# Performance work log

Measured on AMD Instinct MI355X. Metric: run time of the kernel, lower is better.

The kernel has to match this reference:

```python
import jax, jax.numpy as jnp
import numpy as np

B = 32768          # batch (replay-buffer minibatch)
OBS, ACT = 17, 6   # HalfCheetah-style dims
IN = OBS + ACT
H = 256            # hidden width hard-coded in the module
N = 10             # num_q_nets


def setup_inputs() -> dict:
    key = jax.random.key(0)
    ks = jax.random.split(key, 8)
    # PyTorch Linear default init: U(-1/sqrt(fan_in), 1/sqrt(fan_in)); scale randn similarly.
    s1, s2, s3 = 1.0 / np.sqrt(IN), 1.0 / np.sqrt(H), 1.0 / np.sqrt(H)
    return {
        "state": jax.random.normal(ks[0], (B, OBS), dtype=jnp.float32),
        "action": jax.random.uniform(ks[1], (B, ACT), dtype=jnp.float32, minval=-1.0, maxval=1.0),
        "W1": jax.random.normal(ks[2], (N, IN, H), dtype=jnp.float32) * s1,
        "b1": jax.random.normal(ks[3], (N, H), dtype=jnp.float32) * s1,
        "W2": jax.random.normal(ks[4], (N, H, H), dtype=jnp.float32) * s2,
        "b2": jax.random.normal(ks[5], (N, H), dtype=jnp.float32) * s2,
        "W3": jax.random.normal(ks[6], (N, H, 1), dtype=jnp.float32) * s3,
        "b3": jax.random.normal(ks[7], (N, 1), dtype=jnp.float32) * s3,
    }


def reference(state, action, W1, b1, W2, b2, W3, b3):
    # x: [B, OBS+ACT]
    x = jnp.concatenate([state, action], axis=1)
    # batched-over-ensemble GEMMs; n=ensemble member, b=batch
    h1 = jax.nn.relu(jnp.einsum("bi,nih->nbh", x, W1) + b1[:, None, :])   # [N,B,H]
    h2 = jax.nn.relu(jnp.einsum("nbh,nho->nbo", h1, W2) + b2[:, None, :])  # [N,B,H]
    out = jnp.einsum("nbh,nho->nbo", h2, W3) + b3[:, None, :]              # [N,B,1]
    return out
```

## Files before the change

### kernel.cpp

```cpp
#include <hip/hip_runtime.h>
#include <hip/hip_bf16.h>


typedef __attribute__((ext_vector_type(8))) short bf16x8;
typedef __attribute__((ext_vector_type(4))) float f32x4;

#define B_TOTAL 32768
#define NQ 10
#define HDIM 256
#define BT 128
#define XS_STRIDE 40

#define W1P_ELEMS (NQ * 16 * 64 * 8)
#define W2P_ELEMS (NQ * 8 * 16 * 64 * 8)

__device__ __forceinline__ unsigned short f2bf(float f) {
  unsigned int u = __float_as_uint(f);
  u = u + 0x7FFFu + ((u >> 16) & 1u);
  return (unsigned short)(u >> 16);
}

__device__ __forceinline__ unsigned int pk2bf(float a, float b) {
  union { __hip_bfloat162 h; unsigned int u; } cv;
  cv.h = __float22bfloat162_rn(make_float2(a, b));
  return cv.u;
}

__global__ void pack_weights_kernel(const float* __restrict__ W1,
                                    const float* __restrict__ W2,
                                    unsigned short* __restrict__ w1p,
                                    unsigned short* __restrict__ w2p) {
  int t = blockIdx.x * 256 + threadIdx.x;
  const int NW1 = NQ * 16 * 64;
  if (t < NW1) {
    int lane = t & 63, mt = (t >> 6) & 15, n = t >> 10;
    int m = lane & 15, q = lane >> 4;
    int outc = mt * 16 + m;
    unsigned short v[8];
#pragma unroll
    for (int j = 0; j < 8; j++) {
      int k = q * 8 + j;
      v[j] = (k < 23) ? f2bf(W1[(n * 23 + k) * 256 + outc]) : (unsigned short)0;
    }
    *(uint4*)&w1p[(size_t)t * 8] = *(const uint4*)v;
  } else {
    int u = t - NW1;
    int lane = u & 63, mt = (u >> 6) & 15, kt = (u >> 10) & 7, n = u >> 13;
    int m = lane & 15, q = lane >> 4;
    int outc = mt * 16 + m;
    unsigned short v[8];
#pragma unroll
    for (int j = 0; j < 8; j++) {
      int h = kt * 32 + q * 8 + j;
      v[j] = f2bf(W2[((size_t)(n * 256 + h)) * 256 + outc]);
    }
    *(uint4*)&w2p[(size_t)u * 8] = *(const uint4*)v;
  }
}

__global__ __launch_bounds__(512, 4) void fused_ensemble_kernel(
    const float* __restrict__ state,
    const float* __restrict__ action,
    const unsigned short* __restrict__ w1p,
    const float* __restrict__ b1,
    const unsigned short* __restrict__ w2p,
    const float* __restrict__ b2,
    const float* __restrict__ W3,
    const float* __restrict__ b3,
    float* __restrict__ out) {
  __shared__ __align__(16) unsigned short xs[BT * XS_STRIDE];
  __shared__ __align__(16) unsigned short hs[32 * BT * 8];

  const int tid = threadIdx.x;
  const int lane = tid & 63;
  const int w = tid >> 6;
  const int m = lane & 15;
  const int q = lane >> 4;

  const int n = blockIdx.x >> 8;
  const int row0 = (blockIdx.x & 255) * BT;

  {
    const float* sp = state + (size_t)row0 * 17;
    for (int i = tid; i < BT * 17; i += 512) {
      int b = i / 17, k = i - b * 17;
      xs[b * XS_STRIDE + k] = f2bf(sp[i]);
    }
    const float* ap = action + (size_t)row0 * 6;
    for (int i = tid; i < BT * 6; i += 512) {
      int b = i / 6, k = i - b * 6;
      xs[b * XS_STRIDE + 17 + k] = f2bf(ap[i]);
    }
    for (int i = tid; i < BT * 9; i += 512) {
      int b = i / 9, k = i - b * 9;
      xs[b * XS_STRIDE + 23 + k] = 0;
    }
  }
  __syncthreads();

  f32x4 acc[2][8];

  {
    bf16x8 af[2];
#pragma unroll
    for (int mt = 0; mt < 2; mt++)
      af[mt] = *(const bf16x8*)(w1p + (((size_t)n * 16 + w * 2 + mt) * 64 + lane) * 8);
#pragma unroll
    for (int mt = 0; mt < 2; mt++) {
      float4 bv = *(const float4*)&b1[n * HDIM + (w * 2 + mt) * 16 + q * 4];
      f32x4 bi = (f32x4){bv.x, bv.y, bv.z, bv.w};
#pragma unroll
      for (int nt = 0; nt < 8; nt++) acc[mt][nt] = bi;
    }
#pragma unroll
    for (int nt = 0; nt < 8; nt++) {
      bf16x8 bfr = *(const bf16x8*)&xs[(nt * 16 + m) * XS_STRIDE + q * 8];
#pragma unroll
      for (int mt = 0; mt < 2; mt++)
        acc[mt][nt] = __builtin_amdgcn_mfma_f32_16x16x32_bf16(af[mt], bfr, acc[mt][nt], 0, 0, 0);
    }
  }

  {
    const int kqb = w * 4 + (q >> 1);
    const int joff = (q & 1) * 4;
#pragma unroll
    for (int mt = 0; mt < 2; mt++)
#pragma unroll
      for (int nt = 0; nt < 8; nt++) {
        f32x4 a = acc[mt][nt];
        uint2 wv;
        wv.x = pk2bf(fmaxf(a[0], 0.f), fmaxf(a[1], 0.f));
        wv.y = pk2bf(fmaxf(a[2], 0.f), fmaxf(a[3], 0.f));
        *(uint2*)&hs[(((kqb + mt * 2) * BT) + nt * 16 + m) * 8 + joff] = wv;
      }
  }
  __syncthreads();

  {
    const unsigned short* w2n = w2p + (size_t)n * (8 * 16 * 64 * 8);
    bf16x8 acur[2], anxt[2];
#pragma unroll
    for (int mt = 0; mt < 2; mt++)
      acur[mt] = *(const bf16x8*)(w2n + (((size_t)(w * 2 + mt)) * 64 + lane) * 8);
#pragma unroll
    for (int mt = 0; mt < 2; mt++) {
      float4 bv = *(const float4*)&b2[n * HDIM + (w * 2 + mt) * 16 + q * 4];
      f32x4 bi = (f32x4){bv.x, bv.y, bv.z, bv.w};
#pragma unroll
      for (int nt = 0; nt < 8; nt++) acc[mt][nt] = bi;
    }
#pragma unroll
    for (int kt = 0; kt < 8; kt++) {
      if (kt < 7) {
#pragma unroll
        for (int mt = 0; mt < 2; mt++)
          anxt[mt] = *(const bf16x8*)(w2n + (((size_t)(kt + 1) * 16 + w * 2 + mt) * 64 + lane) * 8);
      }
#pragma unroll
      for (int half = 0; half < 2; half++) {
        bf16x8 bfr[4];
#pragma unroll
        for (int i = 0; i < 4; i++) {
          int nt = half * 4 + i;
          bfr[i] = *(const bf16x8*)&hs[((kt * 4 + q) * BT + nt * 16 + m) * 8];
        }
#pragma unroll
        for (int i = 0; i < 4; i++)
#pragma unroll
          for (int mt = 0; mt < 2; mt++)
            acc[mt][half * 4 + i] = __builtin_amdgcn_mfma_f32_16x16x32_bf16(
                acur[mt], bfr[i], acc[mt][half * 4 + i], 0, 0, 0);
      }
#pragma unroll
      for (int mt = 0; mt < 2; mt++) acur[mt] = anxt[mt];
    }
  }

  {
    float4 w3v[2];
#pragma unroll
    for (int mt = 0; mt < 2; mt++)
      w3v[mt] = *(const float4*)&W3[n * HDIM + (w * 2 + mt) * 16 + q * 4];
    float p[8];
#pragma unroll
    for (int nt = 0; nt < 8; nt++) {
      float s = 0.f;
#pragma unroll
      for (int mt = 0; mt < 2; mt++) {
        f32x4 a = acc[mt][nt];
        float4 wv = w3v[mt];
        s = fmaf(fmaxf(a[0], 0.f), wv.x, s);
        s = fmaf(fmaxf(a[1], 0.f), wv.y, s);
        s = fmaf(fmaxf(a[2], 0.f), wv.z, s);
        s = fmaf(fmaxf(a[3], 0.f), wv.w, s);
      }
      s += __shfl_xor(s, 16, 64);
      s += __shfl_xor(s, 32, 64);
      p[nt] = s;
    }
    float* red = (float*)xs;
    if (q == 0) {
#pragma unroll
      for (int nt = 0; nt < 8; nt++) red[w * BT + nt * 16 + m] = p[nt];
    }
    __syncthreads();
    if (tid < BT) {
      float s = b3[n];
#pragma unroll
      for (int ww = 0; ww < 8; ww++) s += red[ww * BT + tid];
      out[(size_t)n * B_TOTAL + row0 + tid] = s;
    }
  }
}

extern "C" void kernel_launch(void* const* d_in, const int* in_sizes, int n_in,
                              void* d_out, int out_size, void* d_ws, size_t ws_size,
                              hipStream_t stream) {
  const float* state  = (const float*)d_in[0];
  const float* action = (const float*)d_in[1];
  const float* W1 = (const float*)d_in[2];
  const float* b1 = (const float*)d_in[3];
  const float* W2 = (const float*)d_in[4];
  const float* b2 = (const float*)d_in[5];
  const float* W3 = (const float*)d_in[6];
  const float* b3 = (const float*)d_in[7];
  float* out = (float*)d_out;

  unsigned short* w1p = (unsigned short*)d_ws;
  unsigned short* w2p = (unsigned short*)((char*)d_ws + (size_t)W1P_ELEMS * 2);

  pack_weights_kernel<<<360, 256, 0, stream>>>(W1, W2, w1p, w2p);
  fused_ensemble_kernel<<<NQ * (B_TOTAL / BT), 512, 0, stream>>>(
      state, action, w1p, b1, w2p, b2, W3, b3, out);
}
```

Baseline: 120.8 us.

## Pre-pack inputs to bf16 and retile waves as 4x4 MFMA blocks

```diff
diff --git a/kernel.cpp b/kernel.cpp
--- a/kernel.cpp
+++ b/kernel.cpp
@@ -9,8 +9,8 @@
 #define NQ 10
 #define HDIM 256
 #define BT 128
-#define XS_STRIDE 40
-
+
+#define XP_ELEMS  (B_TOTAL * 32)
 #define W1P_ELEMS (NQ * 16 * 64 * 8)
 #define W2P_ELEMS (NQ * 8 * 16 * 64 * 8)
 
@@ -26,14 +26,36 @@
   return cv.u;
 }
 
-__global__ void pack_weights_kernel(const float* __restrict__ W1,
-                                    const float* __restrict__ W2,
-                                    unsigned short* __restrict__ w1p,
-                                    unsigned short* __restrict__ w2p) {
+__global__ void pack_all_kernel(const float* __restrict__ state,
+                                const float* __restrict__ action,
+                                const float* __restrict__ W1,
+                                const float* __restrict__ W2,
+                                unsigned short* __restrict__ xp,
+                                unsigned short* __restrict__ w1p,
+                                unsigned short* __restrict__ w2p) {
   int t = blockIdx.x * 256 + threadIdx.x;
+  const int NX  = B_TOTAL * 4;
   const int NW1 = NQ * 16 * 64;
-  if (t < NW1) {
-    int lane = t & 63, mt = (t >> 6) & 15, n = t >> 10;
+  if (t < NX) {
+    int b = t >> 2, seg = t & 3;
+    unsigned short v[8];
+    if (seg < 2) {
+      const float* sp = state + (size_t)b * 17 + seg * 8;
+#pragma unroll
+      for (int j = 0; j < 8; j++) v[j] = f2bf(sp[j]);
+    } else if (seg == 2) {
+      v[0] = f2bf(state[(size_t)b * 17 + 16]);
+#pragma unroll
+      for (int j = 0; j < 6; j++) v[1 + j] = f2bf(action[(size_t)b * 6 + j]);
+      v[7] = 0;
+    } else {
+#pragma unroll
+      for (int j = 0; j < 8; j++) v[j] = 0;
+    }
+    *(uint4*)&xp[(size_t)t * 8] = *(const uint4*)v;
+  } else if (t < NX + NW1) {
+    int u = t - NX;
+    int lane = u & 63, mt = (u >> 6) & 15, n = u >> 10;
     int m = lane & 15, q = lane >> 4;
     int outc = mt * 16 + m;
     unsigned short v[8];
@@ -42,9 +64,9 @@
       int k = q * 8 + j;
       v[j] = (k < 23) ? f2bf(W1[(n * 23 + k) * 256 + outc]) : (unsigned short)0;
     }
-    *(uint4*)&w1p[(size_t)t * 8] = *(const uint4*)v;
+    *(uint4*)&w1p[(size_t)u * 8] = *(const uint4*)v;
   } else {
-    int u = t - NW1;
+    int u = t - NX - NW1;
     int lane = u & 63, mt = (u >> 6) & 15, kt = (u >> 10) & 7, n = u >> 13;
     int m = lane & 15, q = lane >> 4;
     int outc = mt * 16 + m;
@@ -59,8 +81,7 @@
 }
 
 __global__ __launch_bounds__(512, 4) void fused_ensemble_kernel(
-    const float* __restrict__ state,
-    const float* __restrict__ action,
+    const unsigned short* __restrict__ xp,
     const unsigned short* __restrict__ w1p,
     const float* __restrict__ b1,
     const unsigned short* __restrict__ w2p,
@@ -68,126 +89,107 @@
     const float* __restrict__ W3,
     const float* __restrict__ b3,
     float* __restrict__ out) {
-  __shared__ __align__(16) unsigned short xs[BT * XS_STRIDE];
   __shared__ __align__(16) unsigned short hs[32 * BT * 8];
+  __shared__ float red[8 * 64];
 
   const int tid = threadIdx.x;
   const int lane = tid & 63;
   const int w = tid >> 6;
   const int m = lane & 15;
   const int q = lane >> 4;
+  const int cg = w >> 1;
+  const int colg = w & 1;
 
   const int n = blockIdx.x >> 8;
   const int row0 = (blockIdx.x & 255) * BT;
 
+  f32x4 acc[4][4];
+
   {
-    const float* sp = state + (size_t)row0 * 17;
-    for (int i = tid; i < BT * 17; i += 512) {
-      int b = i / 17, k = i - b * 17;
-      xs[b * XS_STRIDE + k] = f2bf(sp[i]);
-    }
-    const float* ap = action + (size_t)row0 * 6;
-    for (int i = tid; i < BT * 6; i += 512) {
-      int b = i / 6, k = i - b * 6;
-      xs[b * XS_STRIDE + 17 + k] = f2bf(ap[i]);
-    }
-    for (int i = tid; i < BT * 9; i += 512) {
-      int b = i / 9, k = i - b * 9;
-      xs[b * XS_STRIDE + 23 + k] = 0;
-    }
-  }
-  __syncthreads();
-
-  f32x4 acc[2][8];
-
-  {
-    bf16x8 af[2];
-#pragma unroll
-    for (int mt = 0; mt < 2; mt++)
-      af[mt] = *(const bf16x8*)(w1p + (((size_t)n * 16 + w * 2 + mt) * 64 + lane) * 8);
-#pragma unroll
-    for (int mt = 0; mt < 2; mt++) {
-      float4 bv = *(const float4*)&b1[n * HDIM + (w * 2 + mt) * 16 + q * 4];
+    bf16x8 af[4], bfr[4];
+#pragma unroll
+    for (int nt = 0; nt < 4; nt++) {
+      int col = row0 + colg * 64 + nt * 16 + m;
+      bfr[nt] = *(const bf16x8*)(xp + (size_t)col * 32 + q * 8);
+    }
+#pragma unroll
+    for (int mt = 0; mt < 4; mt++)
+      af[mt] = *(const bf16x8*)(w1p + (((size_t)n * 16 + cg * 4 + mt) * 64 + lane) * 8);
+#pragma unroll
+    for (int mt = 0; mt < 4; mt++) {
+      float4 bv = *(const float4*)&b1[n * HDIM + (cg * 4 + mt) * 16 + q * 4];
       f32x4 bi = (f32x4){bv.x, bv.y, bv.z, bv.w};
 #pragma unroll
-      for (int nt = 0; nt < 8; nt++) acc[mt][nt] = bi;
-    }
-#pragma unroll
-    for (int nt = 0; nt < 8; nt++) {
-      bf16x8 bfr = *(const bf16x8*)&xs[(nt * 16 + m) * XS_STRIDE + q * 8];
-#pragma unroll
-      for (int mt = 0; mt < 2; mt++)
-        acc[mt][nt] = __builtin_amdgcn_mfma_f32_16x16x32_bf16(af[mt], bfr, acc[mt][nt], 0, 0, 0);
-    }
-  }
-
-  {
-    const int kqb = w * 4 + (q >> 1);
-    const int joff = (q & 1) * 4;
-#pragma unroll
-    for (int mt = 0; mt < 2; mt++)
-#pragma unroll
-      for (int nt = 0; nt < 8; nt++) {
-        f32x4 a = acc[mt][nt];
-        uint2 wv;
-        wv.x = pk2bf(fmaxf(a[0], 0.f), fmaxf(a[1], 0.f));
-        wv.y = pk2bf(fmaxf(a[2], 0.f), fmaxf(a[3], 0.f));
-        *(uint2*)&hs[(((kqb + mt * 2) * BT) + nt * 16 + m) * 8 + joff] = wv;
-      }
+      for (int nt = 0; nt < 4; nt++) acc[mt][nt] = bi;
+    }
+#pragma unroll
+    for (int nt = 0; nt < 4; nt++)
+#pragma unroll
+      for (int mt = 0; mt < 4; mt++)
+        acc[mt][nt] = __builtin_amdgcn_mfma_f32_16x16x32_bf16(af[mt], bfr[nt], acc[mt][nt], 0, 0, 0);
+  }
+
+#pragma unroll
+  for (int mt = 0; mt < 4; mt++) {
+    int kq = cg * 8 + mt * 2 + (q >> 1);
+    int joff = (q & 1) * 4;
+#pragma unroll
+    for (int nt = 0; nt < 4; nt++) {
+      int col = colg * 64 + nt * 16 + m;
+      f32x4 a = acc[mt][nt];
+      uint2 wv;
+      wv.x = pk2bf(fmaxf(a[0], 0.f), fmaxf(a[1], 0.f));
+      wv.y = pk2bf(fmaxf(a[2], 0.f), fmaxf(a[3], 0.f));
+      *(uint2*)&hs[((size_t)kq * BT + col) * 8 + joff] = wv;
+    }
   }
   __syncthreads();
 
   {
     const unsigned short* w2n = w2p + (size_t)n * (8 * 16 * 64 * 8);
-    bf16x8 acur[2], anxt[2];
-#pragma unroll
-    for (int mt = 0; mt < 2; mt++)
-      acur[mt] = *(const bf16x8*)(w2n + (((size_t)(w * 2 + mt)) * 64 + lane) * 8);
-#pragma unroll
-    for (int mt = 0; mt < 2; mt++) {
-      float4 bv = *(const float4*)&b2[n * HDIM + (w * 2 + mt) * 16 + q * 4];
+    bf16x8 acur[4], anxt[4];
+#pragma unroll
+    for (int mt = 0; mt < 4; mt++)
+      acur[mt] = *(const bf16x8*)(w2n + (((size_t)cg * 4 + mt) * 64 + lane) * 8);
+#pragma unroll
+    for (int mt = 0; mt < 4; mt++) {
+      float4 bv = *(const float4*)&b2[n * HDIM + (cg * 4 + mt) * 16 + q * 4];
       f32x4 bi = (f32x4){bv.x, bv.y, bv.z, bv.w};
 #pragma unroll
-      for (int nt = 0; nt < 8; nt++) acc[mt][nt] = bi;
+      for (int nt = 0; nt < 4; nt++) acc[mt][nt] = bi;
     }
 #pragma unroll
     for (int kt = 0; kt < 8; kt++) {
       if (kt < 7) {
 #pragma unroll
-        for (int mt = 0; mt < 2; mt++)
-          anxt[mt] = *(const bf16x8*)(w2n + (((size_t)(kt + 1) * 16 + w * 2 + mt) * 64 + lane) * 8);
+        for (int mt = 0; mt < 4; mt++)
+          anxt[mt] = *(const bf16x8*)(w2n + (((size_t)(kt + 1) * 16 + cg * 4 + mt) * 64 + lane) * 8);
       }
-#pragma unroll
-      for (int half = 0; half < 2; half++) {
-        bf16x8 bfr[4];
-#pragma unroll
-        for (int i = 0; i < 4; i++) {
-          int nt = half * 4 + i;
-          bfr[i] = *(const bf16x8*)&hs[((kt * 4 + q) * BT + nt * 16 + m) * 8];
-        }
-#pragma unroll
-        for (int i = 0; i < 4; i++)
-#pragma unroll
-          for (int mt = 0; mt < 2; mt++)
-            acc[mt][half * 4 + i] = __builtin_amdgcn_mfma_f32_16x16x32_bf16(
-                acur[mt], bfr[i], acc[mt][half * 4 + i], 0, 0, 0);
-      }
-#pragma unroll
-      for (int mt = 0; mt < 2; mt++) acur[mt] = anxt[mt];
+      bf16x8 bfr[4];
+#pragma unroll
+      for (int nt = 0; nt < 4; nt++)
+        bfr[nt] = *(const bf16x8*)&hs[(((size_t)kt * 4 + q) * BT + colg * 64 + nt * 16 + m) * 8];
+#pragma unroll
+      for (int nt = 0; nt < 4; nt++)
+#pragma unroll
+        for (int mt = 0; mt < 4; mt++)
+          acc[mt][nt] = __builtin_amdgcn_mfma_f32_16x16x32_bf16(acur[mt], bfr[nt], acc[mt][nt], 0, 0, 0);
+#pragma unroll
+      for (int mt = 0; mt < 4; mt++) acur[mt] = anxt[mt];
     }
   }
 
   {
-    float4 w3v[2];
-#pragma unroll
-    for (int mt = 0; mt < 2; mt++)
-      w3v[mt] = *(const float4*)&W3[n * HDIM + (w * 2 + mt) * 16 + q * 4];
-    float p[8];
-#pragma unroll
-    for (int nt = 0; nt < 8; nt++) {
+    float4 w3v[4];
+#pragma unroll
+    for (int mt = 0; mt < 4; mt++)
+      w3v[mt] = *(const float4*)&W3[n * HDIM + (cg * 4 + mt) * 16 + q * 4];
+    float p[4];
+#pragma unroll
+    for (int nt = 0; nt < 4; nt++) {
       float s = 0.f;
 #pragma unroll
-      for (int mt = 0; mt < 2; mt++) {
+      for (int mt = 0; mt < 4; mt++) {
         f32x4 a = acc[mt][nt];
         float4 wv = w3v[mt];
         s = fmaf(fmaxf(a[0], 0.f), wv.x, s);
@@ -199,16 +201,16 @@
       s += __shfl_xor(s, 32, 64);
       p[nt] = s;
     }
-    float* red = (float*)xs;
     if (q == 0) {
 #pragma unroll
-      for (int nt = 0; nt < 8; nt++) red[w * BT + nt * 16 + m] = p[nt];
+      for (int nt = 0; nt < 4; nt++) red[w * 64 + nt * 16 + m] = p[nt];
     }
     __syncthreads();
     if (tid < BT) {
+      int g = tid >> 6, lc = tid & 63;
       float s = b3[n];
 #pragma unroll
-      for (int ww = 0; ww < 8; ww++) s += red[ww * BT + tid];
+      for (int c = 0; c < 4; c++) s += red[(c * 2 + g) * 64 + lc];
       out[(size_t)n * B_TOTAL + row0 + tid] = s;
     }
   }
@@ -227,10 +229,11 @@
   const float* b3 = (const float*)d_in[7];
   float* out = (float*)d_out;
 
-  unsigned short* w1p = (unsigned short*)d_ws;
-  unsigned short* w2p = (unsigned short*)((char*)d_ws + (size_t)W1P_ELEMS * 2);
-
-  pack_weights_kernel<<<360, 256, 0, stream>>>(W1, W2, w1p, w2p);
+  unsigned short* xp  = (unsigned short*)d_ws;
+  unsigned short* w1p = (unsigned short*)((char*)d_ws + (size_t)XP_ELEMS * 2);
+  unsigned short* w2p = (unsigned short*)((char*)d_ws + (size_t)(XP_ELEMS + W1P_ELEMS) * 2);
+
+  pack_all_kernel<<<872, 256, 0, stream>>>(state, action, W1, W2, xp, w1p, w2p);
   fused_ensemble_kernel<<<NQ * (B_TOTAL / BT), 512, 0, stream>>>(
-      state, action, w1p, b1, w2p, b2, W3, b3, out);
-}
+      xp, w1p, b1, w2p, b2, W3, b3, out);
+}
```

After: 118.7 us. About the same (-1.8%).
